# Optimization experiments

Measured on AMD Instinct MI355X. Metric: run time of the kernel, lower is better.

Reference implementation:

```python
import jax, jax.numpy as jnp
import numpy as np

EMB = 512       # emb_dim
H = 8           # n_heads
HD = EMB // H   # head_dim = 64
FREQ = 64       # freq_features
PERIOD = 0.1
N = 2048


def setup_inputs() -> dict:
    key = jax.random.key(0)
    ks = jax.random.split(key, 6)
    x = jax.random.normal(ks[0], (1, N, EMB), dtype=jnp.float32)
    v = jax.random.normal(ks[1], (1, N, 3), dtype=jnp.float32)
    vec_map = v / jnp.linalg.norm(v, axis=-1, keepdims=True)  # unit direction vectors
    s_in = 1.0 / np.sqrt(EMB)
    W_qkv = jax.random.normal(ks[2], (EMB, 3 * EMB), dtype=jnp.float32) * s_in
    b_qkv = jnp.zeros((3 * EMB,), dtype=jnp.float32)
    W_bias = jax.random.normal(ks[3], (FREQ, H), dtype=jnp.float32) * (1.0 / np.sqrt(FREQ))
    b_bias = jnp.zeros((H,), dtype=jnp.float32)
    W_out = jax.random.normal(ks[4], (EMB, EMB), dtype=jnp.float32) * s_in
    b_out = jnp.zeros((EMB,), dtype=jnp.float32)
    return {"x": x, "vec_map": vec_map, "W_qkv": W_qkv, "b_qkv": b_qkv,
            "W_bias": W_bias, "b_bias": b_bias, "W_out": W_out, "b_out": b_out}


def reference(x, vec_map, W_qkv, b_qkv, W_bias, b_bias, W_out, b_out):
    batch_dim = x.shape[:-2]
    n = x.shape[-2]
    # QKV projection -> (*, N, H, 3, HD)
    qkv = (x @ W_qkv + b_qkv).reshape(*batch_dim, n, H, 3, HD)
    q, k, v = (qkv[..., 0, :], qkv[..., 1, :], qkv[..., 2, :])
    # attention scores (*, Q, K, H), softmax over the K axis (axis=-2)
    attn = jnp.einsum('...qht,...kht->...qkh', q, k) / np.sqrt(HD)
    attn = jax.nn.softmax(attn, axis=-2)
    # relative bias from pairwise angles between direction vectors
    dot = jnp.einsum('...nc,...mc->...nm', vec_map, vec_map)
    angle = jnp.arccos(jnp.clip(dot, 0.0, 1.0)) / 0.001
    freqs = jnp.linspace(0.0, 1.0, FREQ // 2, dtype=jnp.float32) / PERIOD
    phase = freqs * angle[..., None]                      # (*, N, N, FREQ/2)
    pos = jnp.concatenate((jnp.sin(phase), jnp.cos(phase)), axis=-1)  # (*, N, N, FREQ)
    bias = pos @ W_bias + b_bias                          # (*, N, N, H)
    attn = attn + bias
    # weighted sum of values -> (*, N, EMB)
    y = jnp.einsum('...qkh,...kht->...qht', attn, v).reshape(*batch_dim, n, EMB)
    return y @ W_out + b_out
```

## Files before the change

kernel.cpp:

```cpp
#include <hip/hip_runtime.h>
#include <hip/hip_bf16.h>
#include <math.h>

#define NT 2048
#define EMBD 512
#define NH 8
#define QKV_LD 1536

typedef unsigned short u16;
typedef __attribute__((ext_vector_type(8))) short short8;
typedef __attribute__((ext_vector_type(4))) float v4f;

static __device__ __forceinline__ float bf2f(unsigned int u) {
    union { unsigned int i; float f; } c; c.i = u << 16; return c.f;
}
static __device__ __forceinline__ void unpack4(uint2 r, float* f) {
    f[0] = bf2f(r.x & 0xffffu); f[1] = bf2f(r.x >> 16);
    f[2] = bf2f(r.y & 0xffffu); f[3] = bf2f(r.y >> 16);
}
static __device__ __forceinline__ unsigned int f2bf(float x) {
    union { float f; unsigned int u; } c; c.f = x;
    return (c.u + 0x7fffu + ((c.u >> 16) & 1u)) >> 16;
}

__global__ __launch_bounds__(256) void split_x(const float* __restrict__ x,
    u16* __restrict__ xh, u16* __restrict__ xl)
{
    int i = (blockIdx.x * 256 + threadIdx.x) << 2;
    float4 v = *(const float4*)(x + i);
    float f[4] = {v.x, v.y, v.z, v.w};
    unsigned int hi[4], lo[4];
#pragma unroll
    for (int j = 0; j < 4; ++j) {
        hi[j] = f2bf(f[j]);
        lo[j] = f2bf(f[j] - bf2f(hi[j]));
    }
    uint2 wh; wh.x = hi[0] | (hi[1] << 16); wh.y = hi[2] | (hi[3] << 16);
    uint2 wl; wl.x = lo[0] | (lo[1] << 16); wl.y = lo[2] | (lo[3] << 16);
    *(uint2*)(xh + i) = wh;
    *(uint2*)(xl + i) = wl;
}

__global__ __launch_bounds__(256) void split_wt(const float* __restrict__ W,
    u16* __restrict__ wth, u16* __restrict__ wtl, int ld)
{
    __shared__ float tile[64][65];
    const int n0 = blockIdx.x << 6, k0 = blockIdx.y << 6;
    const int t = threadIdx.x;
    const int r = t >> 2, c4 = (t & 3) << 4;
#pragma unroll
    for (int j = 0; j < 4; ++j)
        *(float4*)&tile[r][c4 + (j << 2)] =
            *(const float4*)(W + (size_t)(k0 + r) * ld + n0 + c4 + (j << 2));
    __syncthreads();
    const int n_l = t >> 2;
    u16 th[16], tl[16];
#pragma unroll
    for (int j = 0; j < 16; ++j) {
        float f = tile[c4 + j][n_l];
        unsigned int h = f2bf(f);
        th[j] = (u16)h;
        tl[j] = (u16)f2bf(f - bf2f(h));
    }
    u16* dh = wth + (size_t)(n0 + n_l) * EMBD + k0 + c4;
    u16* dl = wtl + (size_t)(n0 + n_l) * EMBD + k0 + c4;
    *(uint4*)dh       = *(uint4*)&th[0];
    *(uint4*)(dh + 8) = *(uint4*)&th[8];
    *(uint4*)dl       = *(uint4*)&tl[0];
    *(uint4*)(dl + 8) = *(uint4*)&tl[8];
}

__global__ __launch_bounds__(256) void gemm_qkv_mfma(const u16* __restrict__ xh,
    const u16* __restrict__ xl, const u16* __restrict__ wth,
    const u16* __restrict__ wtl, const float* __restrict__ bias,
    u16* __restrict__ qkvb)
{
    const int n0 = blockIdx.x << 6, m0 = blockIdx.y << 6;
    const int w = threadIdx.x >> 6, lane = threadIdx.x & 63;
    const int wm = w >> 1, wn = w & 1;
    const int fr = lane & 15, kd = (lane >> 4) << 3;

    const u16* ah0 = xh + (size_t)(m0 + wm * 32 + fr) * EMBD + kd;
    const u16* al0 = xl + (size_t)(m0 + wm * 32 + fr) * EMBD + kd;
    const u16* bh0 = wth + (size_t)(n0 + wn * 32 + fr) * EMBD + kd;
    const u16* bl0 = wtl + (size_t)(n0 + wn * 32 + fr) * EMBD + kd;

    v4f acc[2][2] = {};
    for (int kc = 0; kc < EMBD; kc += 32) {
        short8 a_h[2], a_l[2], b_h[2], b_l[2];
#pragma unroll
        for (int im = 0; im < 2; ++im) {
            a_h[im] = *(const short8*)(ah0 + (size_t)im * 16 * EMBD + kc);
            a_l[im] = *(const short8*)(al0 + (size_t)im * 16 * EMBD + kc);
        }
#pragma unroll
        for (int in = 0; in < 2; ++in) {
            b_h[in] = *(const short8*)(bh0 + (size_t)in * 16 * EMBD + kc);
            b_l[in] = *(const short8*)(bl0 + (size_t)in * 16 * EMBD + kc);
        }
#pragma unroll
        for (int im = 0; im < 2; ++im)
#pragma unroll
            for (int in = 0; in < 2; ++in) {
                acc[im][in] = __builtin_amdgcn_mfma_f32_16x16x32_bf16(a_h[im], b_h[in], acc[im][in], 0, 0, 0);
                acc[im][in] = __builtin_amdgcn_mfma_f32_16x16x32_bf16(a_h[im], b_l[in], acc[im][in], 0, 0, 0);
                acc[im][in] = __builtin_amdgcn_mfma_f32_16x16x32_bf16(a_l[im], b_h[in], acc[im][in], 0, 0, 0);
            }
    }
    const int qr = (lane >> 4) << 2;
#pragma unroll
    for (int im = 0; im < 2; ++im)
#pragma unroll
        for (int in = 0; in < 2; ++in) {
            int n = n0 + wn * 32 + in * 16 + fr;
            float bv = bias[n];
#pragma unroll
            for (int r = 0; r < 4; ++r) {
                int m = m0 + wm * 32 + im * 16 + qr + r;
                qkvb[(size_t)m * QKV_LD + n] = (u16)f2bf(acc[im][in][r] + bv);
            }
        }
}

__global__ __launch_bounds__(256) void transpose_v(const u16* __restrict__ qkvb,
                                                   u16* __restrict__ Vt)
{
    __shared__ u16 tile[64][72];
    const int h = blockIdx.y, k0 = blockIdx.x << 6;
    const int t = threadIdx.x;
    {
        int r = t >> 2, cg = (t & 3) << 4;
        const u16* src = qkvb + (size_t)(k0 + r) * QKV_LD + h * 192 + 128 + cg;
        *(uint4*)&tile[r][cg]     = *(const uint4*)src;
        *(uint4*)&tile[r][cg + 8] = *(const uint4*)(src + 8);
    }
    __syncthreads();
    {
        int c = t >> 2, kg = (t & 3) << 4;
        u16 tmp[16];
#pragma unroll
        for (int j = 0; j < 16; ++j) tmp[j] = tile[kg + j][c];
        u16* dst = Vt + ((size_t)h * 64 + c) * NT + k0 + kg;
        *(uint4*)dst       = *(uint4*)&tmp[0];
        *(uint4*)(dst + 8) = *(uint4*)&tmp[8];
    }
}

__global__ __launch_bounds__(256) void scores_mfma(const u16* __restrict__ qkvb,
                                                   u16* __restrict__ s,
                                                   float* __restrict__ zbuf)
{
    __shared__ u16 tile[128][144];
    const int h = blockIdx.z;
    const int kb = blockIdx.x << 7;
    const int qb = blockIdx.y << 7;
    const int w = threadIdx.x >> 6;
    const int q0 = qb + (w << 5);
    const int lane = threadIdx.x & 63;
    const int fr = lane & 15;
    const int kd = (lane >> 4) << 3;

    const u16* qbase = qkvb + (size_t)(q0 + fr) * QKV_LD + h * 192 + kd;
    const u16* kbase = qkvb + (size_t)(kb + fr) * QKV_LD + h * 192 + 64 + kd;

    short8 aq[2][2];
    aq[0][0] = *(const short8*)(qbase);
    aq[0][1] = *(const short8*)(qbase + 32);
    aq[1][0] = *(const short8*)(qbase + (size_t)16 * QKV_LD);
    aq[1][1] = *(const short8*)(qbase + (size_t)16 * QKV_LD + 32);

    v4f acc[2][8] = {};
#pragma unroll
    for (int nt = 0; nt < 8; ++nt) {
        short8 b0 = *(const short8*)(kbase + (size_t)nt * 16 * QKV_LD);
        short8 b1 = *(const short8*)(kbase + (size_t)nt * 16 * QKV_LD + 32);
        acc[0][nt] = __builtin_amdgcn_mfma_f32_16x16x32_bf16(aq[0][0], b0, acc[0][nt], 0, 0, 0);
        acc[0][nt] = __builtin_amdgcn_mfma_f32_16x16x32_bf16(aq[0][1], b1, acc[0][nt], 0, 0, 0);
        acc[1][nt] = __builtin_amdgcn_mfma_f32_16x16x32_bf16(aq[1][0], b0, acc[1][nt], 0, 0, 0);
        acc[1][nt] = __builtin_amdgcn_mfma_f32_16x16x32_bf16(aq[1][1], b1, acc[1][nt], 0, 0, 0);
    }
    const int qr = (lane >> 4) << 2;
#pragma unroll
    for (int i = 0; i < 2; ++i)
#pragma unroll
        for (int nt = 0; nt < 8; ++nt)
#pragma unroll
            for (int r = 0; r < 4; ++r)
                tile[(w << 5) + (i << 4) + qr + r][(nt << 4) + fr] =
                    (u16)f2bf(acc[i][nt][r] * 0.125f);
    float es[2][4];
#pragma unroll
    for (int i = 0; i < 2; ++i)
#pragma unroll
        for (int r = 0; r < 4; ++r) {
            float sum = 0.f;
#pragma unroll
            for (int nt = 0; nt < 8; ++nt)
                sum += __expf(acc[i][nt][r] * 0.125f);
            es[i][r] = sum;
        }
#pragma unroll
    for (int off = 1; off < 16; off <<= 1)
#pragma unroll
        for (int i = 0; i < 2; ++i)
#pragma unroll
            for (int r = 0; r < 4; ++r)
                es[i][r] += __shfl_xor(es[i][r], off);
    if (fr == 0) {
#pragma unroll
        for (int i = 0; i < 2; ++i)
#pragma unroll
            for (int r = 0; r < 4; ++r)
                atomicAdd(zbuf + h * NT + q0 + (i << 4) + qr + r, es[i][r]);
    }
    __syncthreads();
    const int row0 = threadIdx.x >> 4;
    const int col = (threadIdx.x & 15) << 3;
#pragma unroll
    for (int l = 0; l < 8; ++l) {
        int row = row0 + (l << 4);
        *(uint4*)(s + ((size_t)h * NT + qb + row) * NT + kb + col) =
            *(uint4*)&tile[row][col];
    }
}

__global__ __launch_bounds__(256) void bias_kernel(u16* __restrict__ s,
    const float* __restrict__ vec, const float* __restrict__ Wb,
    const float* __restrict__ bb, const float* __restrict__ zbuf)
{
    __shared__ float flds[32];
    __shared__ float vql[96], vkl[96];
    __shared__ float bbl[8];
    __shared__ float ang_lds[1057];
    __shared__ float biasl[8 * 1057];

    const int t = threadIdx.x;
    int b = blockIdx.x, tq = 0, rem = 64;
    while (b >= rem) { b -= rem; ++tq; --rem; }
    const int tk = tq + b;
    const int q0 = tq << 5, k0 = tk << 5;

    if (t < 32) flds[t] = __fdiv_rn(__fdiv_rn((float)t, 31.0f), 0.1f);
    else if (t < 128) vql[t - 32] = vec[q0 * 3 + (t - 32)];
    else if (t < 224) vkl[t - 128] = vec[k0 * 3 + (t - 128)];
    else if (t < 232) bbl[t - 224] = bb[t - 224];
    __syncthreads();

    {
        const int qq = t & 31, kb = (t >> 5) << 2;
        const float a0 = vql[qq * 3], a1 = vql[qq * 3 + 1], a2 = vql[qq * 3 + 2];
#pragma unroll
        for (int j = 0; j < 4; ++j) {
            const int kk = kb + j;
            float c0 = vkl[kk * 3], c1 = vkl[kk * 3 + 1], c2 = vkl[kk * 3 + 2];
            float dot = __fadd_rn(__fadd_rn(__fmul_rn(a0, c0), __fmul_rn(a1, c1)),
                                  __fmul_rn(a2, c2));
            float dotc = fminf(fmaxf(dot, 0.0f), 1.0f);
            ang_lds[qq * 33 + kk] = __fdiv_rn(acosf(dotc), 0.001f);
        }
    }
    __syncthreads();

    {
        const int w = t >> 6, lane = t & 63;
        const int fr = lane & 15, kd = (lane >> 4) << 3, qr = (lane >> 4) << 2;
        short8 BS, BC;
#pragma unroll
        for (int j = 0; j < 8; ++j) {
            float ws = (fr < 8) ? Wb[(kd + j) * 8 + fr] : 0.0f;
            float wc = (fr < 8) ? Wb[(32 + kd + j) * 8 + fr] : 0.0f;
            BS[j] = (short)f2bf(ws);
            BC[j] = (short)f2bf(wc);
        }
        for (int tt = w; tt < 64; tt += 4) {
            int p = (tt << 4) + fr;
            float ang = ang_lds[(p >> 5) * 33 + (p & 31)];
            short8 AS, AC;
#pragma unroll
            for (int j = 0; j < 8; ++j) {
                float ph = __fmul_rn(flds[kd + j], ang);
                float rv = ph * 0.15915494309189535f;
                float rf = rv - floorf(rv);
                AS[j] = (short)f2bf(__builtin_amdgcn_sinf(rf));
                AC[j] = (short)f2bf(__builtin_amdgcn_cosf(rf));
            }
            v4f c = {};
            c = __builtin_amdgcn_mfma_f32_16x16x32_bf16(AS, BS, c, 0, 0, 0);
            c = __builtin_amdgcn_mfma_f32_16x16x32_bf16(AC, BC, c, 0, 0, 0);
            if (fr < 8) {
#pragma unroll
                for (int r = 0; r < 4; ++r) {
                    int pp = (tt << 4) + qr + r;
                    biasl[fr * 1057 + (pp >> 5) * 33 + (pp & 31)] = c[r];
                }
            }
        }
    }
    __syncthreads();

    const int r = t >> 3;
    const int cg = (t & 7) << 2;
    {
        const int q = q0 + r;
#pragma unroll
        for (int h = 0; h < 8; ++h) {
            const float iz = 1.0f / zbuf[h * NT + q];
            const float bv = bbl[h];
            const size_t base = ((size_t)h * NT + q) * NT + k0 + cg;
            uint2 raw = *(const uint2*)(s + base);
            float v[4]; unpack4(raw, v);
            unsigned int o[4];
#pragma unroll
            for (int j = 0; j < 4; ++j) {
                float bias = biasl[h * 1057 + r * 33 + cg + j];
                o[j] = f2bf(__expf(v[j]) * iz + bias + bv);
            }
            uint2 wv; wv.x = o[0] | (o[1] << 16); wv.y = o[2] | (o[3] << 16);
            *(uint2*)(s + base) = wv;
        }
    }
    if (tk != tq) {
        const int q = k0 + r;
#pragma unroll
        for (int h = 0; h < 8; ++h) {
            const float iz = 1.0f / zbuf[h * NT + q];
            const float bv = bbl[h];
            const size_t base = ((size_t)h * NT + q) * NT + q0 + cg;
            uint2 raw = *(const uint2*)(s + base);
            float v[4]; unpack4(raw, v);
            unsigned int o[4];
#pragma unroll
            for (int j = 0; j < 4; ++j) {
                float bias = biasl[h * 1057 + (cg + j) * 33 + r];
                o[j] = f2bf(__expf(v[j]) * iz + bias + bv);
            }
            uint2 wv; wv.x = o[0] | (o[1] << 16); wv.y = o[2] | (o[3] << 16);
            *(uint2*)(s + base) = wv;
        }
    }
}

__global__ __launch_bounds__(256) void attnv_mfma(const u16* __restrict__ attn,
    const u16* __restrict__ Vt, float* __restrict__ ypart)
{
    const int h = blockIdx.y, z = blockIdx.z;
    const int q0 = (blockIdx.x << 6) + ((threadIdx.x >> 6) << 4);
    const int lane = threadIdx.x & 63;
    const int fr = lane & 15;
    const int kd = (lane >> 4) << 3;
    const int kbase = z << 9;

    const u16* arow  = attn + (size_t)(h * NT + q0 + fr) * NT + kbase + kd;
    const u16* vbase = Vt + ((size_t)h * 64 + fr) * NT + kbase + kd;

    v4f c[4] = {};
    for (int ks = 0; ks < 512; ks += 32) {
        short8 a = *(const short8*)(arow + ks);
#pragma unroll
        for (int nt = 0; nt < 4; ++nt) {
            short8 bv = *(const short8*)(vbase + (size_t)nt * 16 * NT + ks);
            c[nt] = __builtin_amdgcn_mfma_f32_16x16x32_bf16(a, bv, c[nt], 0, 0, 0);
        }
    }
    float* yp = ypart + (size_t)z * NT * EMBD;
    const int qr = (lane >> 4) << 2;
#pragma unroll
    for (int nt = 0; nt < 4; ++nt)
#pragma unroll
        for (int r = 0; r < 4; ++r)
            yp[(size_t)(q0 + qr + r) * EMBD + (h << 6) + (nt << 4) + fr] = c[nt][r];
}

__global__ __launch_bounds__(256) void reduce_y(const float* __restrict__ parts,
    u16* __restrict__ yh, u16* __restrict__ yl)
{
    const int MN = NT * EMBD;
    int i = (blockIdx.x * 256 + threadIdx.x) << 2;
    float4 acc = *(const float4*)(parts + i);
#pragma unroll
    for (int sp = 1; sp < 4; ++sp) {
        float4 p = *(const float4*)(parts + (size_t)sp * MN + i);
        acc.x += p.x; acc.y += p.y; acc.z += p.z; acc.w += p.w;
    }
    float f[4] = {acc.x, acc.y, acc.z, acc.w};
    unsigned int hi[4], lo[4];
#pragma unroll
    for (int j = 0; j < 4; ++j) {
        hi[j] = f2bf(f[j]);
        lo[j] = f2bf(f[j] - bf2f(hi[j]));
    }
    uint2 wh; wh.x = hi[0] | (hi[1] << 16); wh.y = hi[2] | (hi[3] << 16);
    uint2 wl; wl.x = lo[0] | (lo[1] << 16); wl.y = lo[2] | (lo[3] << 16);
    *(uint2*)(yh + i) = wh;
    *(uint2*)(yl + i) = wl;
}

__global__ __launch_bounds__(256) void gemm_out_mfma(const u16* __restrict__ yh,
    const u16* __restrict__ yl, const u16* __restrict__ wh,
    const u16* __restrict__ wl, const float* __restrict__ bias,
    float* __restrict__ out)
{
    const int n0 = blockIdx.x << 6, m0 = blockIdx.y << 6;
    const int w = threadIdx.x >> 6, lane = threadIdx.x & 63;
    const int wm = w >> 1, wn = w & 1;
    const int fr = lane & 15, kd = (lane >> 4) << 3;

    const u16* ah0 = yh + (size_t)(m0 + wm * 32 + fr) * EMBD + kd;
    const u16* al0 = yl + (size_t)(m0 + wm * 32 + fr) * EMBD + kd;
    const u16* bh0 = wh + (size_t)(n0 + wn * 32 + fr) * EMBD + kd;
    const u16* bl0 = wl + (size_t)(n0 + wn * 32 + fr) * EMBD + kd;

    v4f acc[2][2] = {};
    for (int kc = 0; kc < EMBD; kc += 32) {
        short8 a_h[2], a_l[2], b_h[2], b_l[2];
#pragma unroll
        for (int im = 0; im < 2; ++im) {
            a_h[im] = *(const short8*)(ah0 + (size_t)im * 16 * EMBD + kc);
            a_l[im] = *(const short8*)(al0 + (size_t)im * 16 * EMBD + kc);
        }
#pragma unroll
        for (int in = 0; in < 2; ++in) {
            b_h[in] = *(const short8*)(bh0 + (size_t)in * 16 * EMBD + kc);
            b_l[in] = *(const short8*)(bl0 + (size_t)in * 16 * EMBD + kc);
        }
#pragma unroll
        for (int im = 0; im < 2; ++im)
#pragma unroll
            for (int in = 0; in < 2; ++in) {
                acc[im][in] = __builtin_amdgcn_mfma_f32_16x16x32_bf16(a_h[im], b_h[in], acc[im][in], 0, 0, 0);
                acc[im][in] = __builtin_amdgcn_mfma_f32_16x16x32_bf16(a_h[im], b_l[in], acc[im][in], 0, 0, 0);
                acc[im][in] = __builtin_amdgcn_mfma_f32_16x16x32_bf16(a_l[im], b_h[in], acc[im][in], 0, 0, 0);
            }
    }
    const int qr = (lane >> 4) << 2;
#pragma unroll
    for (int im = 0; im < 2; ++im)
#pragma unroll
        for (int in = 0; in < 2; ++in) {
            int n = n0 + wn * 32 + in * 16 + fr;
            float bv = bias[n];
#pragma unroll
            for (int r = 0; r < 4; ++r) {
                int m = m0 + wm * 32 + im * 16 + qr + r;
                out[(size_t)m * EMBD + n] = acc[im][in][r] + bv;
            }
        }
}

extern "C" void kernel_launch(void* const* d_in, const int* in_sizes, int n_in,
                              void* d_out, int out_size, void* d_ws, size_t ws_size,
                              hipStream_t stream)
{
    const float* x    = (const float*)d_in[0];
    const float* vec  = (const float*)d_in[1];
    const float* Wqkv = (const float*)d_in[2];
    const float* bqkv = (const float*)d_in[3];
    const float* Wb   = (const float*)d_in[4];
    const float* bb   = (const float*)d_in[5];
    const float* Wout = (const float*)d_in[6];
    const float* bout = (const float*)d_in[7];
    float* out = (float*)d_out;

    char* ws = (char*)d_ws;
    u16*   qkvb  = (u16*)(ws);
    u16*   sbuf  = (u16*)(ws + 6291456);
    u16*   Vt    = (u16*)(ws + 73400320);
    float* zbuf  = (float*)(ws + 75497472);
    u16*   yh    = (u16*)(ws + 75628544);
    u16*   yl    = (u16*)(ws + 77725696);
    float* parts = (float*)(ws + 79822848);
    u16*   xh    = (u16*)(ws + 79822848);
    u16*   xl    = (u16*)(ws + 81920000);
    u16*   wth   = (u16*)(ws + 84017152);
    u16*   wtl   = (u16*)(ws + 85590016);
    u16*   woth  = (u16*)(ws + 79822848);
    u16*   wotl  = (u16*)(ws + 80347136);

    hipMemsetAsync(zbuf, 0, NH * NT * sizeof(float), stream);
    split_x<<<1024, 256, 0, stream>>>(x, xh, xl);
    split_wt<<<dim3(24, 8), 256, 0, stream>>>(Wqkv, wth, wtl, QKV_LD);
    gemm_qkv_mfma<<<dim3(24, 32), 256, 0, stream>>>(xh, xl, wth, wtl, bqkv, qkvb);
    transpose_v<<<dim3(32, 8), 256, 0, stream>>>(qkvb, Vt);
    scores_mfma<<<dim3(16, 16, 8), 256, 0, stream>>>(qkvb, sbuf, zbuf);
    bias_kernel<<<2080, 256, 0, stream>>>(sbuf, vec, Wb, bb, zbuf);
    attnv_mfma<<<dim3(32, 8, 4), 256, 0, stream>>>(sbuf, Vt, parts);
    reduce_y<<<1024, 256, 0, stream>>>(parts, yh, yl);
    split_wt<<<dim3(8, 8), 256, 0, stream>>>(Wout, woth, wotl, EMBD);
    gemm_out_mfma<<<dim3(8, 32), 256, 0, stream>>>(yh, yl, woth, wotl, bout, out);
}
```

Before: 274.6 us.

## Fuse scores, softmax and AV into flash-style kernel; apply bias via separate GEMM

Measured after the change: 423.8 us. 1.54x slower.

```diff
diff --git a/kernel.cpp b/kernel.cpp
--- a/kernel.cpp
+++ b/kernel.cpp
@@ -13,10 +13,6 @@
 
 static __device__ __forceinline__ float bf2f(unsigned int u) {
     union { unsigned int i; float f; } c; c.i = u << 16; return c.f;
-}
-static __device__ __forceinline__ void unpack4(uint2 r, float* f) {
-    f[0] = bf2f(r.x & 0xffffu); f[1] = bf2f(r.x >> 16);
-    f[2] = bf2f(r.y & 0xffffu); f[3] = bf2f(r.y >> 16);
 }
 static __device__ __forceinline__ unsigned int f2bf(float x) {
     union { float f; unsigned int u; } c; c.f = x;
@@ -146,87 +142,92 @@
     }
 }
 
-__global__ __launch_bounds__(256) void scores_mfma(const u16* __restrict__ qkvb,
-                                                   u16* __restrict__ s,
-                                                   float* __restrict__ zbuf)
-{
-    __shared__ u16 tile[128][144];
-    const int h = blockIdx.z;
-    const int kb = blockIdx.x << 7;
-    const int qb = blockIdx.y << 7;
-    const int w = threadIdx.x >> 6;
-    const int q0 = qb + (w << 5);
-    const int lane = threadIdx.x & 63;
-    const int fr = lane & 15;
-    const int kd = (lane >> 4) << 3;
-
-    const u16* qbase = qkvb + (size_t)(q0 + fr) * QKV_LD + h * 192 + kd;
-    const u16* kbase = qkvb + (size_t)(kb + fr) * QKV_LD + h * 192 + 64 + kd;
-
-    short8 aq[2][2];
-    aq[0][0] = *(const short8*)(qbase);
-    aq[0][1] = *(const short8*)(qbase + 32);
-    aq[1][0] = *(const short8*)(qbase + (size_t)16 * QKV_LD);
-    aq[1][1] = *(const short8*)(qbase + (size_t)16 * QKV_LD + 32);
-
-    v4f acc[2][8] = {};
-#pragma unroll
-    for (int nt = 0; nt < 8; ++nt) {
-        short8 b0 = *(const short8*)(kbase + (size_t)nt * 16 * QKV_LD);
-        short8 b1 = *(const short8*)(kbase + (size_t)nt * 16 * QKV_LD + 32);
-        acc[0][nt] = __builtin_amdgcn_mfma_f32_16x16x32_bf16(aq[0][0], b0, acc[0][nt], 0, 0, 0);
-        acc[0][nt] = __builtin_amdgcn_mfma_f32_16x16x32_bf16(aq[0][1], b1, acc[0][nt], 0, 0, 0);
-        acc[1][nt] = __builtin_amdgcn_mfma_f32_16x16x32_bf16(aq[1][0], b0, acc[1][nt], 0, 0, 0);
-        acc[1][nt] = __builtin_amdgcn_mfma_f32_16x16x32_bf16(aq[1][1], b1, acc[1][nt], 0, 0, 0);
-    }
-    const int qr = (lane >> 4) << 2;
-#pragma unroll
-    for (int i = 0; i < 2; ++i)
-#pragma unroll
-        for (int nt = 0; nt < 8; ++nt)
-#pragma unroll
-            for (int r = 0; r < 4; ++r)
-                tile[(w << 5) + (i << 4) + qr + r][(nt << 4) + fr] =
-                    (u16)f2bf(acc[i][nt][r] * 0.125f);
-    float es[2][4];
-#pragma unroll
-    for (int i = 0; i < 2; ++i)
-#pragma unroll
-        for (int r = 0; r < 4; ++r) {
-            float sum = 0.f;
-#pragma unroll
-            for (int nt = 0; nt < 8; ++nt)
-                sum += __expf(acc[i][nt][r] * 0.125f);
-            es[i][r] = sum;
-        }
+__global__ __launch_bounds__(256) void flash_attn(const u16* __restrict__ qkvb,
+    const u16* __restrict__ Vt, float* __restrict__ numpart,
+    float* __restrict__ zpart)
+{
+    __shared__ u16 P[4][2][16][40];
+    const int h = blockIdx.y, z = blockIdx.z;
+    const int w = threadIdx.x >> 6, lane = threadIdx.x & 63;
+    const int fr = lane & 15, kd = (lane >> 4) << 3, qr = (lane >> 4) << 2;
+    const int q0 = (blockIdx.x << 6) + (w << 4);
+    const int kbase = z << 9;
+
+    const u16* qb = qkvb + (size_t)(q0 + fr) * QKV_LD + h * 192 + kd;
+    short8 qa0 = *(const short8*)(qb);
+    short8 qa1 = *(const short8*)(qb + 32);
+    const u16* kbp = qkvb + (size_t)kbase * QKV_LD + h * 192 + 64 + kd;
+    const u16* vb  = Vt + ((size_t)h * 64 + fr) * NT + kbase + kd;
+
+    v4f acc[4] = {};
+    float zac[4] = {};
+    int buf = 0;
+    for (int kt = 0; kt < 512; kt += 32) {
+#pragma unroll
+        for (int ks = 0; ks < 2; ++ks) {
+            const u16* kr = kbp + (size_t)(kt + ks * 16 + fr) * QKV_LD;
+            short8 kb0 = *(const short8*)(kr);
+            short8 kb1 = *(const short8*)(kr + 32);
+            v4f c = {};
+            c = __builtin_amdgcn_mfma_f32_16x16x32_bf16(qa0, kb0, c, 0, 0, 0);
+            c = __builtin_amdgcn_mfma_f32_16x16x32_bf16(qa1, kb1, c, 0, 0, 0);
+#pragma unroll
+            for (int r = 0; r < 4; ++r) {
+                float ex = __expf(c[r] * 0.125f);
+                zac[r] += ex;
+                P[w][buf][qr + r][ks * 16 + fr] = (u16)f2bf(ex);
+            }
+        }
+        __syncthreads();
+        union { uint2 u2[2]; short8 s8; } pa;
+        pa.u2[0] = *(uint2*)&P[w][buf][fr][kd];
+        pa.u2[1] = *(uint2*)&P[w][buf][fr][kd + 4];
+#pragma unroll
+        for (int ti = 0; ti < 4; ++ti) {
+            short8 bfr = *(const short8*)(vb + (size_t)(ti * 16) * NT + kt);
+            acc[ti] = __builtin_amdgcn_mfma_f32_16x16x32_bf16(pa.s8, bfr, acc[ti], 0, 0, 0);
+        }
+        buf ^= 1;
+    }
 #pragma unroll
     for (int off = 1; off < 16; off <<= 1)
 #pragma unroll
-        for (int i = 0; i < 2; ++i)
-#pragma unroll
-            for (int r = 0; r < 4; ++r)
-                es[i][r] += __shfl_xor(es[i][r], off);
+        for (int r = 0; r < 4; ++r) zac[r] += __shfl_xor(zac[r], off);
     if (fr == 0) {
 #pragma unroll
-        for (int i = 0; i < 2; ++i)
-#pragma unroll
-            for (int r = 0; r < 4; ++r)
-                atomicAdd(zbuf + h * NT + q0 + (i << 4) + qr + r, es[i][r]);
-    }
-    __syncthreads();
-    const int row0 = threadIdx.x >> 4;
-    const int col = (threadIdx.x & 15) << 3;
-#pragma unroll
-    for (int l = 0; l < 8; ++l) {
-        int row = row0 + (l << 4);
-        *(uint4*)(s + ((size_t)h * NT + qb + row) * NT + kb + col) =
-            *(uint4*)&tile[row][col];
-    }
-}
-
-__global__ __launch_bounds__(256) void bias_kernel(u16* __restrict__ s,
-    const float* __restrict__ vec, const float* __restrict__ Wb,
-    const float* __restrict__ bb, const float* __restrict__ zbuf)
+        for (int r = 0; r < 4; ++r)
+            zpart[((size_t)z * NH + h) * NT + q0 + qr + r] = zac[r];
+    }
+    float* np = numpart + (size_t)z * NT * EMBD;
+#pragma unroll
+    for (int ti = 0; ti < 4; ++ti)
+#pragma unroll
+        for (int r = 0; r < 4; ++r)
+            np[(size_t)(q0 + qr + r) * EMBD + (h << 6) + (ti << 4) + fr] = acc[ti][r];
+}
+
+__global__ __launch_bounds__(256) void combine_num(const float* __restrict__ numpart,
+    const float* __restrict__ zpart, float* __restrict__ y1)
+{
+    int i = (blockIdx.x * 256 + threadIdx.x) << 2;
+    const int q = i >> 9, h = (i & 511) >> 6;
+    float zs = 0.f;
+#pragma unroll
+    for (int z = 0; z < 4; ++z) zs += zpart[((size_t)z * NH + h) * NT + q];
+    const float inv = 1.0f / zs;
+    float4 a = *(const float4*)(numpart + i);
+#pragma unroll
+    for (int z = 1; z < 4; ++z) {
+        float4 p = *(const float4*)(numpart + (size_t)z * NT * EMBD + i);
+        a.x += p.x; a.y += p.y; a.z += p.z; a.w += p.w;
+    }
+    a.x *= inv; a.y *= inv; a.z *= inv; a.w *= inv;
+    *(float4*)(y1 + i) = a;
+}
+
+__global__ __launch_bounds__(256) void bias_bv(const float* __restrict__ vec,
+    const float* __restrict__ Wb, const float* __restrict__ bb,
+    const u16* __restrict__ Vt, float* __restrict__ y1)
 {
     __shared__ float flds[32];
     __shared__ float vql[96], vkl[96];
@@ -298,91 +299,52 @@
     }
     __syncthreads();
 
-    const int r = t >> 3;
-    const int cg = (t & 7) << 2;
     {
-        const int q = q0 + r;
-#pragma unroll
-        for (int h = 0; h < 8; ++h) {
-            const float iz = 1.0f / zbuf[h * NT + q];
+        const int w = t >> 6, lane = t & 63;
+        const int fr = lane & 15, kd8 = (lane >> 4) << 3, qr = (lane >> 4) << 2;
+        for (int u = w; u < 16; u += 4) {
+            const int h = u >> 1, o = u & 1;
+            if (o && tk == tq) continue;
             const float bv = bbl[h];
-            const size_t base = ((size_t)h * NT + q) * NT + k0 + cg;
-            uint2 raw = *(const uint2*)(s + base);
-            float v[4]; unpack4(raw, v);
-            unsigned int o[4];
-#pragma unroll
-            for (int j = 0; j < 4; ++j) {
-                float bias = biasl[h * 1057 + r * 33 + cg + j];
-                o[j] = f2bf(__expf(v[j]) * iz + bias + bv);
-            }
-            uint2 wv; wv.x = o[0] | (o[1] << 16); wv.y = o[2] | (o[3] << 16);
-            *(uint2*)(s + base) = wv;
-        }
-    }
-    if (tk != tq) {
-        const int q = k0 + r;
-#pragma unroll
-        for (int h = 0; h < 8; ++h) {
-            const float iz = 1.0f / zbuf[h * NT + q];
-            const float bv = bbl[h];
-            const size_t base = ((size_t)h * NT + q) * NT + q0 + cg;
-            uint2 raw = *(const uint2*)(s + base);
-            float v[4]; unpack4(raw, v);
-            unsigned int o[4];
-#pragma unroll
-            for (int j = 0; j < 4; ++j) {
-                float bias = biasl[h * 1057 + (cg + j) * 33 + r];
-                o[j] = f2bf(__expf(v[j]) * iz + bias + bv);
-            }
-            uint2 wv; wv.x = o[0] | (o[1] << 16); wv.y = o[2] | (o[3] << 16);
-            *(uint2*)(s + base) = wv;
-        }
-    }
-}
-
-__global__ __launch_bounds__(256) void attnv_mfma(const u16* __restrict__ attn,
-    const u16* __restrict__ Vt, float* __restrict__ ypart)
-{
-    const int h = blockIdx.y, z = blockIdx.z;
-    const int q0 = (blockIdx.x << 6) + ((threadIdx.x >> 6) << 4);
-    const int lane = threadIdx.x & 63;
-    const int fr = lane & 15;
-    const int kd = (lane >> 4) << 3;
-    const int kbase = z << 9;
-
-    const u16* arow  = attn + (size_t)(h * NT + q0 + fr) * NT + kbase + kd;
-    const u16* vbase = Vt + ((size_t)h * 64 + fr) * NT + kbase + kd;
-
-    v4f c[4] = {};
-    for (int ks = 0; ks < 512; ks += 32) {
-        short8 a = *(const short8*)(arow + ks);
-#pragma unroll
-        for (int nt = 0; nt < 4; ++nt) {
-            short8 bv = *(const short8*)(vbase + (size_t)nt * 16 * NT + ks);
-            c[nt] = __builtin_amdgcn_mfma_f32_16x16x32_bf16(a, bv, c[nt], 0, 0, 0);
-        }
-    }
-    float* yp = ypart + (size_t)z * NT * EMBD;
-    const int qr = (lane >> 4) << 2;
-#pragma unroll
-    for (int nt = 0; nt < 4; ++nt)
-#pragma unroll
-        for (int r = 0; r < 4; ++r)
-            yp[(size_t)(q0 + qr + r) * EMBD + (h << 6) + (nt << 4) + fr] = c[nt][r];
-}
-
-__global__ __launch_bounds__(256) void reduce_y(const float* __restrict__ parts,
+            short8 afr[2];
+#pragma unroll
+            for (int mi = 0; mi < 2; ++mi) {
+                short8 a;
+#pragma unroll
+                for (int j = 0; j < 8; ++j) {
+                    float val = (o == 0)
+                        ? biasl[h * 1057 + (mi * 16 + fr) * 33 + kd8 + j] + bv
+                        : biasl[h * 1057 + (kd8 + j) * 33 + mi * 16 + fr] + bv;
+                    a[j] = (short)f2bf(val);
+                }
+                afr[mi] = a;
+            }
+            const int vrow0 = (o == 0) ? k0 : q0;
+            const int orow0 = (o == 0) ? q0 : k0;
+            const u16* vb = Vt + ((size_t)h * 64) * NT + vrow0 + kd8;
+#pragma unroll
+            for (int ti = 0; ti < 4; ++ti) {
+                short8 bfr = *(const short8*)(vb + (size_t)(ti * 16 + fr) * NT);
+#pragma unroll
+                for (int mi = 0; mi < 2; ++mi) {
+                    v4f c = {};
+                    c = __builtin_amdgcn_mfma_f32_16x16x32_bf16(afr[mi], bfr, c, 0, 0, 0);
+#pragma unroll
+                    for (int r = 0; r < 4; ++r)
+                        atomicAdd(y1 + (size_t)(orow0 + mi * 16 + qr + r) * EMBD +
+                                  (h << 6) + (ti << 4) + fr, c[r]);
+                }
+            }
+        }
+    }
+}
+
+__global__ __launch_bounds__(256) void conv_y(const float* __restrict__ y1,
     u16* __restrict__ yh, u16* __restrict__ yl)
 {
-    const int MN = NT * EMBD;
     int i = (blockIdx.x * 256 + threadIdx.x) << 2;
-    float4 acc = *(const float4*)(parts + i);
-#pragma unroll
-    for (int sp = 1; sp < 4; ++sp) {
-        float4 p = *(const float4*)(parts + (size_t)sp * MN + i);
-        acc.x += p.x; acc.y += p.y; acc.z += p.z; acc.w += p.w;
-    }
-    float f[4] = {acc.x, acc.y, acc.z, acc.w};
+    float4 v = *(const float4*)(y1 + i);
+    float f[4] = {v.x, v.y, v.z, v.w};
     unsigned int hi[4], lo[4];
 #pragma unroll
     for (int j = 0; j < 4; ++j) {
@@ -463,28 +425,27 @@
 
     char* ws = (char*)d_ws;
     u16*   qkvb  = (u16*)(ws);
-    u16*   sbuf  = (u16*)(ws + 6291456);
-    u16*   Vt    = (u16*)(ws + 73400320);
-    float* zbuf  = (float*)(ws + 75497472);
-    u16*   yh    = (u16*)(ws + 75628544);
-    u16*   yl    = (u16*)(ws + 77725696);
-    float* parts = (float*)(ws + 79822848);
-    u16*   xh    = (u16*)(ws + 79822848);
-    u16*   xl    = (u16*)(ws + 81920000);
-    u16*   wth   = (u16*)(ws + 84017152);
-    u16*   wtl   = (u16*)(ws + 85590016);
-    u16*   woth  = (u16*)(ws + 79822848);
-    u16*   wotl  = (u16*)(ws + 80347136);
-
-    hipMemsetAsync(zbuf, 0, NH * NT * sizeof(float), stream);
+    u16*   Vt    = (u16*)(ws + 6291456);
+    float* zpart = (float*)(ws + 8388608);
+    float* y1    = (float*)(ws + 8650752);
+    u16*   yh    = (u16*)(ws + 12845056);
+    u16*   yl    = (u16*)(ws + 14942208);
+    float* nump  = (float*)(ws + 17039360);
+    u16*   xh    = (u16*)(ws + 33816576);
+    u16*   xl    = (u16*)(ws + 35913728);
+    u16*   wth   = (u16*)(ws + 38010880);
+    u16*   wtl   = (u16*)(ws + 39583744);
+    u16*   woth  = (u16*)(ws + 41156608);
+    u16*   wotl  = (u16*)(ws + 41680896);
+
     split_x<<<1024, 256, 0, stream>>>(x, xh, xl);
     split_wt<<<dim3(24, 8), 256, 0, stream>>>(Wqkv, wth, wtl, QKV_LD);
     gemm_qkv_mfma<<<dim3(24, 32), 256, 0, stream>>>(xh, xl, wth, wtl, bqkv, qkvb);
     transpose_v<<<dim3(32, 8), 256, 0, stream>>>(qkvb, Vt);
-    scores_mfma<<<dim3(16, 16, 8), 256, 0, stream>>>(qkvb, sbuf, zbuf);
-    bias_kernel<<<2080, 256, 0, stream>>>(sbuf, vec, Wb, bb, zbuf);
-    attnv_mfma<<<dim3(32, 8, 4), 256, 0, stream>>>(sbuf, Vt, parts);
-    reduce_y<<<1024, 256, 0, stream>>>(parts, yh, yl);
+    flash_attn<<<dim3(32, 8, 4), 256, 0, stream>>>(qkvb, Vt, nump, zpart);
+    combine_num<<<1024, 256, 0, stream>>>(nump, zpart, y1);
+    bias_bv<<<2080, 256, 0, stream>>>(vec, Wb, bb, Vt, y1);
+    conv_y<<<1024, 256, 0, stream>>>(y1, yh, yl);
     split_wt<<<dim3(8, 8), 256, 0, stream>>>(Wout, woth, wotl, EMBD);
     gemm_out_mfma<<<dim3(8, 32), 256, 0, stream>>>(yh, yl, woth, wotl, bout, out);
 }
```
